# Kernel optimization log

Hardware: AMD Instinct MI355X
Metric: run time of the kernel (lower is better)

Reference implementation:

```python
import jax, jax.numpy as jnp
import numpy as np

HEADS = 2
HID = 128
IN_DIM = 128
OUT_DIM = 1
N_NODES = 50000
NEG_SLOPE = 0.2  # PyG GATConv default
EPS = 1e-16


def setup_inputs() -> dict:
    key = jax.random.key(0)
    ks = jax.random.split(key, 16)
    N, E = N_NODES, 800000
    x = jax.random.normal(ks[0], (N, IN_DIM), dtype=jnp.float32)
    edge_index = jax.random.randint(ks[1], (2, E), 0, N, dtype=jnp.int32)
    s = 0.1
    # GATConv 1: in=128 -> heads=2, out=128 per head
    W1 = jax.random.normal(ks[2], (IN_DIM, HEADS * HID), dtype=jnp.float32) * s
    a_src1 = jax.random.normal(ks[3], (HEADS, HID), dtype=jnp.float32) * s
    a_dst1 = jax.random.normal(ks[4], (HEADS, HID), dtype=jnp.float32) * s
    b1 = jnp.zeros((HEADS * HID,), dtype=jnp.float32)
    # GATConv 2: in=256 -> heads=2, out=128 per head
    W2 = jax.random.normal(ks[5], (HEADS * HID, HEADS * HID), dtype=jnp.float32) * s
    a_src2 = jax.random.normal(ks[6], (HEADS, HID), dtype=jnp.float32) * s
    a_dst2 = jax.random.normal(ks[7], (HEADS, HID), dtype=jnp.float32) * s
    b2 = jnp.zeros((HEADS * HID,), dtype=jnp.float32)
    # post_mp: Linear(256,128) -> Dropout -> Linear(128,1)
    Wp1 = jax.random.normal(ks[8], (HEADS * HID, HID), dtype=jnp.float32) * s
    bp1 = jnp.zeros((HID,), dtype=jnp.float32)
    Wp2 = jax.random.normal(ks[9], (HID, OUT_DIM), dtype=jnp.float32) * s
    bp2 = jnp.zeros((OUT_DIM,), dtype=jnp.float32)
    return {"x": x, "edge_index": edge_index,
            "W1": W1, "a_src1": a_src1, "a_dst1": a_dst1, "b1": b1,
            "W2": W2, "a_src2": a_src2, "a_dst2": a_dst2, "b2": b2,
            "Wp1": Wp1, "bp1": bp1, "Wp2": Wp2, "bp2": bp2}


def gat_conv(x, src, dst, W, a_src, a_dst, b, num_nodes):
    """PyG-style GATConv (concat=True). src/dst already include self-loops."""
    N = num_nodes
    h = (x @ W).reshape(N, HEADS, HID)                        # [N,H,C]
    alpha_s = jnp.einsum('nhc,hc->nh', h, a_src)              # [N,H]
    alpha_d = jnp.einsum('nhc,hc->nh', h, a_dst)              # [N,H]
    e = jax.nn.leaky_relu(alpha_s[src] + alpha_d[dst], NEG_SLOPE)  # [E,H]
    # segment softmax over destination node
    emax = jax.ops.segment_max(e, dst, num_segments=N)        # [N,H]
    emax = jnp.where(jnp.isfinite(emax), emax, 0.0)
    w = jnp.exp(e - emax[dst])                                # [E,H]
    denom = jax.ops.segment_sum(w, dst, num_segments=N)       # [N,H]
    alpha = w / (denom[dst] + EPS)                            # [E,H]
    out = jax.ops.segment_sum(h[src] * alpha[:, :, None], dst, num_segments=N)
    return out.reshape(N, HEADS * HID) + b


def reference(x, edge_index, W1, a_src1, a_dst1, b1, W2, a_src2, a_dst2, b2,
              Wp1, bp1, Wp2, bp2):
    N = x.shape[0]
    loops = jnp.arange(N, dtype=edge_index.dtype)
    src = jnp.concatenate([edge_index[0], loops])
    dst = jnp.concatenate([edge_index[1], loops])
    h = gat_conv(x, src, dst, W1, a_src1, a_dst1, b1, N)
    h = jax.nn.relu(h)  # dropout is identity in eval mode
    h = gat_conv(h, src, dst, W2, a_src2, a_dst2, b2, N)
    h = jax.nn.relu(h)
    h = h @ Wp1 + bp1
    h = h @ Wp2 + bp2
    return jax.nn.sigmoid(h)
```

## Files before the change

kernel.cpp:

```cpp
#include <hip/hip_runtime.h>

#define HID 128
#define C2 256
#define NEG 0.2f
#define L2E 1.44269504088896340736f

typedef __bf16 v8bf __attribute__((ext_vector_type(8)));
typedef float  v4f  __attribute__((ext_vector_type(4)));
typedef float  v2f  __attribute__((ext_vector_type(2)));
typedef unsigned short us8 __attribute__((ext_vector_type(8)));

__device__ __forceinline__ float bf2f(unsigned short u) {
    union { float f; unsigned int i; } v; v.i = ((unsigned int)u) << 16; return v.f;
}
__device__ __forceinline__ unsigned short f2bf(float f) {
    union { float f; unsigned int i; } v; v.f = f;
    unsigned int r = v.i + 0x7FFFu + ((v.i >> 16) & 1u);
    return (unsigned short)(r >> 16);
}
__device__ __forceinline__ float lrelu(float x) { return x > 0.f ? x : NEG * x; }

__device__ __forceinline__ void packB_body(const float* __restrict__ W,
                                           unsigned short* __restrict__ out,
                                           int K, int N, int idx) {
    int ksteps = K >> 5;
    int total = (N >> 4) * ksteps * 64;
    if (idx >= total) return;
    int lane = idx & 63;
    int rest = idx >> 6;
    int tt = rest / ksteps, k0 = rest - tt * ksteps;
    int n = (tt >> 3) * 128 + (lane & 15) * 8 + (tt & 7);
    int kb = k0 * 32 + (lane >> 4) * 8;
    us8 v;
#pragma unroll
    for (int j = 0; j < 8; ++j) v[j] = f2bf(W[(size_t)(kb + j) * N + n]);
    *(us8*)(out + (size_t)idx * 8) = v;
}

__global__ __launch_bounds__(256) void prep_kernel(const float* __restrict__ W1, unsigned short* W1p,
                                                   const float* __restrict__ W2, unsigned short* W2p,
                                                   const float* __restrict__ Wp1, unsigned short* Wp1p,
                                                   const int* __restrict__ ei, int* __restrict__ cnt,
                                                   int* __restrict__ rank, int E,
                                                   int b1, int b2, int b3) {
    int b = blockIdx.x;
    if (b < b1) { packB_body(W1, W1p, HID, C2, b * 256 + threadIdx.x); return; }
    b -= b1;
    if (b < b2) { packB_body(W2, W2p, C2, C2, b * 256 + threadIdx.x); return; }
    b -= b2;
    if (b < b3) { packB_body(Wp1, Wp1p, C2, HID, b * 256 + threadIdx.x); return; }
    b -= b3;
    int i = b * 256 + threadIdx.x;
    if (i >= E) return;
    int d = ei[E + i];
    rank[i] = atomicAdd(&cnt[d], 1);
}

__global__ __launch_bounds__(256) void scanA(const int* __restrict__ cnt, int* __restrict__ rs,
                                             int* __restrict__ part, int N) {
    __shared__ int s[256];
    int t = threadIdx.x, i = blockIdx.x * 256 + t;
    int v = (i < N) ? cnt[i] : 0;
    s[t] = v; __syncthreads();
    for (int off = 1; off < 256; off <<= 1) {
        int x = (t >= off) ? s[t - off] : 0;
        __syncthreads();
        s[t] += x;
        __syncthreads();
    }
    if (i < N) rs[i] = s[t] - v;
    if (t == 255) part[blockIdx.x] = s[255];
}

__global__ __launch_bounds__(256) void scanB(int* __restrict__ part, int n) {
    __shared__ int s[256];
    int t = threadIdx.x;
    int v = (t < n) ? part[t] : 0;
    s[t] = v; __syncthreads();
    for (int off = 1; off < 256; off <<= 1) {
        int x = (t >= off) ? s[t - off] : 0;
        __syncthreads();
        s[t] += x;
        __syncthreads();
    }
    if (t < n) part[t] = s[t] - v;
}

__global__ void scanC(int* __restrict__ rs, const int* __restrict__ part, int N, int E) {
    int i = blockIdx.x * 256 + threadIdx.x;
    if (i < N) rs[i] += part[blockIdx.x];
    if (i == 0) rs[N] = E;
}

template<bool AFP32, int G, int KSTEPS>
__global__ __launch_bounds__(256) void gemm_alpha(const void* __restrict__ Av,
                                                  const unsigned short* __restrict__ Bp,
                                                  const float* __restrict__ asrc,
                                                  const float* __restrict__ adst,
                                                  float* __restrict__ asd,
                                                  unsigned char* __restrict__ C,
                                                  int M, int N, int gemmBlocks,
                                                  const int* __restrict__ ei,
                                                  const int* __restrict__ rs,
                                                  const int* __restrict__ rank,
                                                  int* __restrict__ csr, int E) {
    if (blockIdx.x >= gemmBlocks) {
        int i = (blockIdx.x - gemmBlocks) * 256 + threadIdx.x;
        if (i < E) {
            int s = ei[i], d = ei[E + i];
            csr[rs[d] + rank[i]] = s;
        }
        return;
    }
    constexpr int K = KSTEPS * 32;
    int ngrp = N >> 7;
    int mtiles = M >> 4;
    int w = (blockIdx.x << 2) + (threadIdx.x >> 6);
    int groups = (mtiles + G - 1) / G;
    int mp = w / ngrp, g = w - mp * ngrp;
    if (mp >= groups) return;
    int lane = threadIdx.x & 63;
    int l16 = lane & 15, quad = lane >> 4;
    int mt0 = mp * G;

    int mrow[G];
#pragma unroll
    for (int gi = 0; gi < G; ++gi) {
        int mt = mt0 + gi;
        mrow[gi] = (mt < mtiles ? mt : mtiles - 1) * 16 + l16;
    }

    const unsigned short* Bf = Bp + ((size_t)(g * 8) * KSTEPS << 9) + lane * 8;
    v4f acc[G][8];
#pragma unroll
    for (int gi = 0; gi < G; ++gi)
#pragma unroll
        for (int t = 0; t < 8; ++t) acc[gi][t] = (v4f){0, 0, 0, 0};

#pragma unroll
    for (int k0 = 0; k0 < KSTEPS; ++k0) {
        v8bf bfr[8];
#pragma unroll
        for (int t = 0; t < 8; ++t)
            bfr[t] = *(const v8bf*)(Bf + ((size_t)(t * KSTEPS + k0) << 9));
        v8bf a[G];
        if (AFP32) {
            const float* A = (const float*)Av;
#pragma unroll
            for (int gi = 0; gi < G; ++gi) {
                const float* p = A + (size_t)mrow[gi] * K + k0 * 32 + quad * 8;
                float4 u0 = *(const float4*)p, u1 = *(const float4*)(p + 4);
                a[gi][0]=(__bf16)u0.x; a[gi][1]=(__bf16)u0.y; a[gi][2]=(__bf16)u0.z; a[gi][3]=(__bf16)u0.w;
                a[gi][4]=(__bf16)u1.x; a[gi][5]=(__bf16)u1.y; a[gi][6]=(__bf16)u1.z; a[gi][7]=(__bf16)u1.w;
            }
        } else {
            const unsigned short* A = (const unsigned short*)Av;
#pragma unroll
            for (int gi = 0; gi < G; ++gi)
                a[gi] = *(const v8bf*)(A + (size_t)mrow[gi] * K + k0 * 32 + quad * 8);
        }
#pragma unroll
        for (int t = 0; t < 8; ++t)
#pragma unroll
            for (int gi = 0; gi < G; ++gi)
                acc[gi][t] = __builtin_amdgcn_mfma_f32_16x16x32_bf16(a[gi], bfr[t], acc[gi][t], 0, 0, 0);
    }

    int n0 = g << 7;
    int cb = n0 + l16 * 8;
    float sv[8], dv[8];
#pragma unroll
    for (int t = 0; t < 8; ++t) {
        sv[t] = asrc[cb + t];
        dv[t] = adst[cb + t];
    }
#pragma unroll
    for (int gi = 0; gi < G; ++gi) {
        int mt = mt0 + gi;
        if (mt >= mtiles) break;
        int row0 = mt * 16 + quad * 4;
#pragma unroll
        for (int r = 0; r < 4; ++r) {
            float sa = 0.f, sd = 0.f;
#pragma unroll
            for (int t = 0; t < 8; ++t) {
                sa += acc[gi][t][r] * sv[t];
                sd += acc[gi][t][r] * dv[t];
            }
            unsigned int w0 = __builtin_amdgcn_cvt_pk_fp8_f32(acc[gi][0][r], acc[gi][1][r], 0, false);
            w0 = __builtin_amdgcn_cvt_pk_fp8_f32(acc[gi][2][r], acc[gi][3][r], w0, true);
            unsigned int w1 = __builtin_amdgcn_cvt_pk_fp8_f32(acc[gi][4][r], acc[gi][5][r], 0, false);
            w1 = __builtin_amdgcn_cvt_pk_fp8_f32(acc[gi][6][r], acc[gi][7][r], w1, true);
            *(uint2*)(C + (size_t)(row0 + r) * N + cb) = (uint2){w0, w1};
#pragma unroll
            for (int off = 8; off; off >>= 1) {
                sa += __shfl_xor(sa, off);
                sd += __shfl_xor(sd, off);
            }
            if (l16 == 0) {
                int row = row0 + r;
                asd[(size_t)row * 4 + g]     = sa * L2E;
                asd[(size_t)row * 4 + 2 + g] = sd * L2E;
            }
        }
    }
}

__global__ __launch_bounds__(256) void agg_kernel(const int* __restrict__ rs,
                                                  const int* __restrict__ csr,
                                                  const unsigned char* __restrict__ h,
                                                  const float* __restrict__ asd,
                                                  const float* __restrict__ bias,
                                                  unsigned short* __restrict__ out, int N) {
    int tid = threadIdx.x;
    int grp = tid >> 4;
    int sub = tid & 15;
    int d = blockIdx.x * 16 + grp;
    if (d >= N) return;
    int head = sub >> 3;
    int beg = rs[d], end = rs[d + 1];
    float adh = asd[(size_t)d * 4 + 2 + head];
    int cbase = sub * 16;
    const unsigned char* hc = h + cbase;
    v2f acc[8];
#pragma unroll
    for (int j = 0; j < 8; ++j) acc[j] = (v2f){0, 0};
    float den = 0.f;
#pragma unroll 2
    for (int i = beg; i < end; ++i) {
        int s = csr[i];
        float wgt = __builtin_amdgcn_exp2f(lrelu(asd[(size_t)s * 4 + head] + adh));
        den += wgt;
        uint4 u = *(const uint4*)(hc + ((size_t)s << 8));
        v2f w2 = {wgt, wgt};
        acc[0] += w2 * __builtin_amdgcn_cvt_pk_f32_fp8(u.x, false);
        acc[1] += w2 * __builtin_amdgcn_cvt_pk_f32_fp8(u.x, true);
        acc[2] += w2 * __builtin_amdgcn_cvt_pk_f32_fp8(u.y, false);
        acc[3] += w2 * __builtin_amdgcn_cvt_pk_f32_fp8(u.y, true);
        acc[4] += w2 * __builtin_amdgcn_cvt_pk_f32_fp8(u.z, false);
        acc[5] += w2 * __builtin_amdgcn_cvt_pk_f32_fp8(u.z, true);
        acc[6] += w2 * __builtin_amdgcn_cvt_pk_f32_fp8(u.w, false);
        acc[7] += w2 * __builtin_amdgcn_cvt_pk_f32_fp8(u.w, true);
    }
    float wS = __builtin_amdgcn_exp2f(lrelu(asd[(size_t)d * 4 + head] + adh));
    {
        uint4 u = *(const uint4*)(hc + ((size_t)d << 8));
        v2f wsv = {wS, wS};
        acc[0] += wsv * __builtin_amdgcn_cvt_pk_f32_fp8(u.x, false);
        acc[1] += wsv * __builtin_amdgcn_cvt_pk_f32_fp8(u.x, true);
        acc[2] += wsv * __builtin_amdgcn_cvt_pk_f32_fp8(u.y, false);
        acc[3] += wsv * __builtin_amdgcn_cvt_pk_f32_fp8(u.y, true);
        acc[4] += wsv * __builtin_amdgcn_cvt_pk_f32_fp8(u.z, false);
        acc[5] += wsv * __builtin_amdgcn_cvt_pk_f32_fp8(u.z, true);
        acc[6] += wsv * __builtin_amdgcn_cvt_pk_f32_fp8(u.w, false);
        acc[7] += wsv * __builtin_amdgcn_cvt_pk_f32_fp8(u.w, true);
    }
    float rden = 1.f / (den + wS + 1e-16f);
    us8 o0, o1;
#pragma unroll
    for (int j = 0; j < 4; ++j) {
        o0[2 * j]     = f2bf(fmaxf(acc[j].x * rden + bias[cbase + 2 * j], 0.f));
        o0[2 * j + 1] = f2bf(fmaxf(acc[j].y * rden + bias[cbase + 2 * j + 1], 0.f));
        o1[2 * j]     = f2bf(fmaxf(acc[4 + j].x * rden + bias[cbase + 8 + 2 * j], 0.f));
        o1[2 * j + 1] = f2bf(fmaxf(acc[4 + j].y * rden + bias[cbase + 8 + 2 * j + 1], 0.f));
    }
    *(us8*)(out + (size_t)d * C2 + cbase) = o0;
    *(us8*)(out + (size_t)d * C2 + cbase + 8) = o1;
}

template<int G, int KSTEPS>
__global__ __launch_bounds__(256) void gemm_final(const unsigned short* __restrict__ A,
                                                  const unsigned short* __restrict__ Bp,
                                                  const float* __restrict__ bp1,
                                                  const float* __restrict__ wp2,
                                                  const float* __restrict__ bp2,
                                                  float* __restrict__ out,
                                                  int M) {
    constexpr int K = KSTEPS * 32;
    int mtiles = M >> 4;
    int groups = (mtiles + G - 1) / G;
    int mp = (blockIdx.x << 2) + (threadIdx.x >> 6);
    if (mp >= groups) return;
    int lane = threadIdx.x & 63;
    int l16 = lane & 15, quad = lane >> 4;

    int mrow[G];
#pragma unroll
    for (int gi = 0; gi < G; ++gi) {
        int mt = mp * G + gi;
        mrow[gi] = (mt < mtiles ? mt : mtiles - 1) * 16 + l16;
    }

    const unsigned short* Bf = Bp + lane * 8;
    v4f acc[G][8];
#pragma unroll
    for (int gi = 0; gi < G; ++gi)
#pragma unroll
        for (int t = 0; t < 8; ++t) acc[gi][t] = (v4f){0, 0, 0, 0};
#pragma unroll
    for (int k0 = 0; k0 < KSTEPS; ++k0) {
        v8bf bfr[8];
#pragma unroll
        for (int t = 0; t < 8; ++t)
            bfr[t] = *(const v8bf*)(Bf + ((size_t)(t * KSTEPS + k0) << 9));
        v8bf a[G];
#pragma unroll
        for (int gi = 0; gi < G; ++gi)
            a[gi] = *(const v8bf*)(A + (size_t)mrow[gi] * K + k0 * 32 + quad * 8);
#pragma unroll
        for (int t = 0; t < 8; ++t)
#pragma unroll
            for (int gi = 0; gi < G; ++gi)
                acc[gi][t] = __builtin_amdgcn_mfma_f32_16x16x32_bf16(a[gi], bfr[t], acc[gi][t], 0, 0, 0);
    }
    int cb = l16 * 8;
    float wv8[8], bv[8];
#pragma unroll
    for (int t = 0; t < 8; ++t) {
        wv8[t] = wp2[cb + t];
        bv[t] = bp1[cb + t];
    }
    float bias2 = bp2[0];
#pragma unroll
    for (int gi = 0; gi < G; ++gi) {
        int mt = mp * G + gi;
        if (mt >= mtiles) break;
        int row0 = mt * 16 + quad * 4;
#pragma unroll
        for (int r = 0; r < 4; ++r) {
            float s = 0.f;
#pragma unroll
            for (int t = 0; t < 8; ++t) s += (acc[gi][t][r] + bv[t]) * wv8[t];
#pragma unroll
            for (int off = 8; off; off >>= 1) s += __shfl_xor(s, off);
            if (l16 == 0) {
                float xv = s + bias2;
                out[row0 + r] = 1.f / (1.f + __expf(-xv));
            }
        }
    }
}

extern "C" void kernel_launch(void* const* d_in, const int* in_sizes, int n_in,
                              void* d_out, int out_size, void* d_ws, size_t ws_size,
                              hipStream_t stream) {
    const float* x   = (const float*)d_in[0];
    const int*   ei  = (const int*)d_in[1];
    const float* W1  = (const float*)d_in[2];
    const float* as1 = (const float*)d_in[3];
    const float* ad1 = (const float*)d_in[4];
    const float* b1  = (const float*)d_in[5];
    const float* W2  = (const float*)d_in[6];
    const float* as2 = (const float*)d_in[7];
    const float* ad2 = (const float*)d_in[8];
    const float* b2  = (const float*)d_in[9];
    const float* Wp1 = (const float*)d_in[10];
    const float* bp1 = (const float*)d_in[11];
    const float* Wp2 = (const float*)d_in[12];
    const float* bp2 = (const float*)d_in[13];
    float* out = (float*)d_out;

    int NN = in_sizes[0] / HID;
    int E  = in_sizes[1] / 2;

    char* ws = (char*)d_ws;
    size_t off = 0;
    auto alloc = [&](size_t bytes) -> char* {
        char* p = ws + off;
        off += (bytes + 255) & ~(size_t)255;
        return p;
    };
    unsigned char*  bufH = (unsigned char*)alloc((size_t)NN * C2);
    unsigned short* bufO = (unsigned short*)alloc((size_t)NN * C2 * 2);
    float* asd = (float*)alloc((size_t)NN * 4 * sizeof(float));
    int* rs    = (int*)alloc((size_t)(NN + 1) * 4);
    int* cnt   = (int*)alloc((size_t)NN * 4);
    int* rank  = (int*)alloc((size_t)E * 4);
    int* csr   = (int*)alloc((size_t)E * 4);
    int* part  = (int*)alloc(1024);
    unsigned short* W1p  = (unsigned short*)alloc((size_t)HID * C2 * 2);
    unsigned short* W2p  = (unsigned short*)alloc((size_t)C2 * C2 * 2);
    unsigned short* Wp1p = (unsigned short*)alloc((size_t)C2 * HID * 2);

    int nchunk = (NN + 255) / 256;
    int eblk   = (E + 255) / 256;

    int pb1 = (HID * C2 / 8 + 255) / 256;
    int pb2 = (C2 * C2 / 8 + 255) / 256;
    int pb3 = (C2 * HID / 8 + 255) / 256;
    hipMemsetAsync(cnt, 0, (size_t)NN * 4, stream);
    prep_kernel<<<pb1 + pb2 + pb3 + eblk, 256, 0, stream>>>(W1, W1p, W2, W2p, Wp1, Wp1p,
                                                            ei, cnt, rank, E, pb1, pb2, pb3);
    scanA<<<nchunk, 256, 0, stream>>>(cnt, rs, part, NN);
    scanB<<<1, 256, 0, stream>>>(part, nchunk);
    scanC<<<nchunk, 256, 0, stream>>>(rs, part, NN, E);

    const int G = 2;
    int mtiles = NN / 16;
    int groups = (mtiles + G - 1) / G;
    int gemmBlocks = (groups * 2 + 3) / 4;
    int aggGrid = (NN + 15) / 16;

    gemm_alpha<true, G, 4><<<gemmBlocks + eblk, 256, 0, stream>>>(x, W1p, as1, ad1, asd, bufH,
                                                                  NN, C2, gemmBlocks,
                                                                  ei, rs, rank, csr, E);
    agg_kernel<<<aggGrid, 256, 0, stream>>>(rs, csr, bufH, asd, b1, bufO, NN);
    gemm_alpha<false, G, 8><<<gemmBlocks, 256, 0, stream>>>(bufO, W2p, as2, ad2, asd, bufH,
                                                            NN, C2, gemmBlocks,
                                                            nullptr, nullptr, nullptr, nullptr, 0);
    agg_kernel<<<aggGrid, 256, 0, stream>>>(rs, csr, bufH, asd, b2, bufO, NN);
    gemm_final<G, 8><<<(groups + 3) / 4, 256, 0, stream>>>(bufO, Wp1p, bp1, Wp2, bp2, out, NN);
}
```

Measured before the change: 298.1 us.

## Fuse GAT aggregation into following GEMMs via LDS and single-block scan

Each aggregation now writes its 64-row bf16 output tile to shared memory, and the next GEMM (layer-2 projection or the final MLP) consumes it in the same kernel. This removes the global round trip of the intermediate node features and two kernel launches. Separate buffers are used for the layer 1 and layer 2 features and attention scalars. The three-kernel prefix scan is replaced with one 1024-thread block doing a chunked serial scan, which cuts launches but serialises per-thread work and re-reads the counts.

```diff
diff --git a/kernel.cpp b/kernel.cpp
--- a/kernel.cpp
+++ b/kernel.cpp
@@ -56,40 +56,30 @@
     rank[i] = atomicAdd(&cnt[d], 1);
 }
 
-__global__ __launch_bounds__(256) void scanA(const int* __restrict__ cnt, int* __restrict__ rs,
-                                             int* __restrict__ part, int N) {
-    __shared__ int s[256];
-    int t = threadIdx.x, i = blockIdx.x * 256 + t;
-    int v = (i < N) ? cnt[i] : 0;
-    s[t] = v; __syncthreads();
-    for (int off = 1; off < 256; off <<= 1) {
-        int x = (t >= off) ? s[t - off] : 0;
+__global__ __launch_bounds__(1024) void scan_one(const int* __restrict__ cnt,
+                                                 int* __restrict__ rs, int N, int E) {
+    __shared__ int ls[1024];
+    int t = threadIdx.x;
+    int ch = (N + 1023) >> 10;
+    int base = t * ch;
+    int sum = 0;
+    for (int i = 0; i < ch; ++i) {
+        int idx = base + i;
+        sum += (idx < N) ? cnt[idx] : 0;
+    }
+    ls[t] = sum; __syncthreads();
+    for (int off = 1; off < 1024; off <<= 1) {
+        int x = (t >= off) ? ls[t - off] : 0;
         __syncthreads();
-        s[t] += x;
+        ls[t] += x;
         __syncthreads();
     }
-    if (i < N) rs[i] = s[t] - v;
-    if (t == 255) part[blockIdx.x] = s[255];
-}
-
-__global__ __launch_bounds__(256) void scanB(int* __restrict__ part, int n) {
-    __shared__ int s[256];
-    int t = threadIdx.x;
-    int v = (t < n) ? part[t] : 0;
-    s[t] = v; __syncthreads();
-    for (int off = 1; off < 256; off <<= 1) {
-        int x = (t >= off) ? s[t - off] : 0;
-        __syncthreads();
-        s[t] += x;
-        __syncthreads();
-    }
-    if (t < n) part[t] = s[t] - v;
-}
-
-__global__ void scanC(int* __restrict__ rs, const int* __restrict__ part, int N, int E) {
-    int i = blockIdx.x * 256 + threadIdx.x;
-    if (i < N) rs[i] += part[blockIdx.x];
-    if (i == 0) rs[N] = E;
+    int run = ls[t] - sum;
+    for (int i = 0; i < ch; ++i) {
+        int idx = base + i;
+        if (idx < N) { rs[idx] = run; run += cnt[idx]; }
+    }
+    if (t == 1023) rs[N] = E;
 }
 
 template<bool AFP32, int G, int KSTEPS>
@@ -206,97 +196,114 @@
     }
 }
 
-__global__ __launch_bounds__(256) void agg_kernel(const int* __restrict__ rs,
-                                                  const int* __restrict__ csr,
-                                                  const unsigned char* __restrict__ h,
-                                                  const float* __restrict__ asd,
-                                                  const float* __restrict__ bias,
-                                                  unsigned short* __restrict__ out, int N) {
-    int tid = threadIdx.x;
+__device__ __forceinline__ void agg_to_lds(const int* __restrict__ rs,
+                                           const int* __restrict__ csr,
+                                           const unsigned char* __restrict__ h,
+                                           const float* __restrict__ asd,
+                                           const float* __restrict__ bias,
+                                           unsigned short* __restrict__ sA,
+                                           int rowbase, int M, int tid) {
     int grp = tid >> 4;
     int sub = tid & 15;
-    int d = blockIdx.x * 16 + grp;
-    if (d >= N) return;
     int head = sub >> 3;
-    int beg = rs[d], end = rs[d + 1];
-    float adh = asd[(size_t)d * 4 + 2 + head];
     int cbase = sub * 16;
     const unsigned char* hc = h + cbase;
-    v2f acc[8];
-#pragma unroll
-    for (int j = 0; j < 8; ++j) acc[j] = (v2f){0, 0};
-    float den = 0.f;
+    for (int p = 0; p < 4; ++p) {
+        int d = rowbase + p * 16 + grp;
+        if (d >= M) continue;
+        int beg = rs[d], end = rs[d + 1];
+        float adh = asd[(size_t)d * 4 + 2 + head];
+        v2f acc[8];
+#pragma unroll
+        for (int j = 0; j < 8; ++j) acc[j] = (v2f){0, 0};
+        float den = 0.f;
 #pragma unroll 2
-    for (int i = beg; i < end; ++i) {
-        int s = csr[i];
-        float wgt = __builtin_amdgcn_exp2f(lrelu(asd[(size_t)s * 4 + head] + adh));
-        den += wgt;
-        uint4 u = *(const uint4*)(hc + ((size_t)s << 8));
-        v2f w2 = {wgt, wgt};
-        acc[0] += w2 * __builtin_amdgcn_cvt_pk_f32_fp8(u.x, false);
-        acc[1] += w2 * __builtin_amdgcn_cvt_pk_f32_fp8(u.x, true);
-        acc[2] += w2 * __builtin_amdgcn_cvt_pk_f32_fp8(u.y, false);
-        acc[3] += w2 * __builtin_amdgcn_cvt_pk_f32_fp8(u.y, true);
-        acc[4] += w2 * __builtin_amdgcn_cvt_pk_f32_fp8(u.z, false);
-        acc[5] += w2 * __builtin_amdgcn_cvt_pk_f32_fp8(u.z, true);
-        acc[6] += w2 * __builtin_amdgcn_cvt_pk_f32_fp8(u.w, false);
-        acc[7] += w2 * __builtin_amdgcn_cvt_pk_f32_fp8(u.w, true);
-    }
-    float wS = __builtin_amdgcn_exp2f(lrelu(asd[(size_t)d * 4 + head] + adh));
-    {
-        uint4 u = *(const uint4*)(hc + ((size_t)d << 8));
-        v2f wsv = {wS, wS};
-        acc[0] += wsv * __builtin_amdgcn_cvt_pk_f32_fp8(u.x, false);
-        acc[1] += wsv * __builtin_amdgcn_cvt_pk_f32_fp8(u.x, true);
-        acc[2] += wsv * __builtin_amdgcn_cvt_pk_f32_fp8(u.y, false);
-        acc[3] += wsv * __builtin_amdgcn_cvt_pk_f32_fp8(u.y, true);
-        acc[4] += wsv * __builtin_amdgcn_cvt_pk_f32_fp8(u.z, false);
-        acc[5] += wsv * __builtin_amdgcn_cvt_pk_f32_fp8(u.z, true);
-        acc[6] += wsv * __builtin_amdgcn_cvt_pk_f32_fp8(u.w, false);
-        acc[7] += wsv * __builtin_amdgcn_cvt_pk_f32_fp8(u.w, true);
-    }
-    float rden = 1.f / (den + wS + 1e-16f);
-    us8 o0, o1;
-#pragma unroll
-    for (int j = 0; j < 4; ++j) {
-        o0[2 * j]     = f2bf(fmaxf(acc[j].x * rden + bias[cbase + 2 * j], 0.f));
-        o0[2 * j + 1] = f2bf(fmaxf(acc[j].y * rden + bias[cbase + 2 * j + 1], 0.f));
-        o1[2 * j]     = f2bf(fmaxf(acc[4 + j].x * rden + bias[cbase + 8 + 2 * j], 0.f));
-        o1[2 * j + 1] = f2bf(fmaxf(acc[4 + j].y * rden + bias[cbase + 8 + 2 * j + 1], 0.f));
-    }
-    *(us8*)(out + (size_t)d * C2 + cbase) = o0;
-    *(us8*)(out + (size_t)d * C2 + cbase + 8) = o1;
-}
-
-template<int G, int KSTEPS>
-__global__ __launch_bounds__(256) void gemm_final(const unsigned short* __restrict__ A,
-                                                  const unsigned short* __restrict__ Bp,
-                                                  const float* __restrict__ bp1,
-                                                  const float* __restrict__ wp2,
-                                                  const float* __restrict__ bp2,
-                                                  float* __restrict__ out,
-                                                  int M) {
-    constexpr int K = KSTEPS * 32;
+        for (int i = beg; i < end; ++i) {
+            int s = csr[i];
+            float wgt = __builtin_amdgcn_exp2f(lrelu(asd[(size_t)s * 4 + head] + adh));
+            den += wgt;
+            uint4 u = *(const uint4*)(hc + ((size_t)s << 8));
+            v2f w2 = {wgt, wgt};
+            acc[0] += w2 * __builtin_amdgcn_cvt_pk_f32_fp8(u.x, false);
+            acc[1] += w2 * __builtin_amdgcn_cvt_pk_f32_fp8(u.x, true);
+            acc[2] += w2 * __builtin_amdgcn_cvt_pk_f32_fp8(u.y, false);
+            acc[3] += w2 * __builtin_amdgcn_cvt_pk_f32_fp8(u.y, true);
+            acc[4] += w2 * __builtin_amdgcn_cvt_pk_f32_fp8(u.z, false);
+            acc[5] += w2 * __builtin_amdgcn_cvt_pk_f32_fp8(u.z, true);
+            acc[6] += w2 * __builtin_amdgcn_cvt_pk_f32_fp8(u.w, false);
+            acc[7] += w2 * __builtin_amdgcn_cvt_pk_f32_fp8(u.w, true);
+        }
+        float wS = __builtin_amdgcn_exp2f(lrelu(asd[(size_t)d * 4 + head] + adh));
+        {
+            uint4 u = *(const uint4*)(hc + ((size_t)d << 8));
+            v2f wsv = {wS, wS};
+            acc[0] += wsv * __builtin_amdgcn_cvt_pk_f32_fp8(u.x, false);
+            acc[1] += wsv * __builtin_amdgcn_cvt_pk_f32_fp8(u.x, true);
+            acc[2] += wsv * __builtin_amdgcn_cvt_pk_f32_fp8(u.y, false);
+            acc[3] += wsv * __builtin_amdgcn_cvt_pk_f32_fp8(u.y, true);
+            acc[4] += wsv * __builtin_amdgcn_cvt_pk_f32_fp8(u.z, false);
+            acc[5] += wsv * __builtin_amdgcn_cvt_pk_f32_fp8(u.z, true);
+            acc[6] += wsv * __builtin_amdgcn_cvt_pk_f32_fp8(u.w, false);
+            acc[7] += wsv * __builtin_amdgcn_cvt_pk_f32_fp8(u.w, true);
+        }
+        float rden = 1.f / (den + wS + 1e-16f);
+        us8 o0, o1;
+#pragma unroll
+        for (int j = 0; j < 4; ++j) {
+            o0[2 * j]     = f2bf(fmaxf(acc[j].x * rden + bias[cbase + 2 * j], 0.f));
+            o0[2 * j + 1] = f2bf(fmaxf(acc[j].y * rden + bias[cbase + 2 * j + 1], 0.f));
+            o1[2 * j]     = f2bf(fmaxf(acc[4 + j].x * rden + bias[cbase + 8 + 2 * j], 0.f));
+            o1[2 * j + 1] = f2bf(fmaxf(acc[4 + j].y * rden + bias[cbase + 8 + 2 * j + 1], 0.f));
+        }
+        unsigned short* dst = sA + (size_t)(p * 16 + grp) * C2 + cbase;
+        *(us8*)dst = o0;
+        *(us8*)(dst + 8) = o1;
+    }
+}
+
+template<int KSTEPS>
+__global__ __launch_bounds__(256) void agg_gemm_alpha(const int* __restrict__ rs,
+                                                      const int* __restrict__ csr,
+                                                      const unsigned char* __restrict__ hIn,
+                                                      const float* __restrict__ asdIn,
+                                                      const float* __restrict__ biasIn,
+                                                      const unsigned short* __restrict__ Bp,
+                                                      const float* __restrict__ asrc,
+                                                      const float* __restrict__ adst,
+                                                      float* __restrict__ asdOut,
+                                                      unsigned char* __restrict__ C,
+                                                      int M, int N) {
+    __shared__ __align__(16) unsigned short sA[64 * C2];
+    int tid = threadIdx.x;
+    int rowbase = blockIdx.x * 64;
+    agg_to_lds(rs, csr, hIn, asdIn, biasIn, sA, rowbase, M, tid);
+    __syncthreads();
+
+    constexpr int G = 2;
+    int ngrp = N >> 7;
     int mtiles = M >> 4;
+    int w = (blockIdx.x << 2) + (tid >> 6);
     int groups = (mtiles + G - 1) / G;
-    int mp = (blockIdx.x << 2) + (threadIdx.x >> 6);
+    int mp = w / ngrp, g = w - mp * ngrp;
     if (mp >= groups) return;
-    int lane = threadIdx.x & 63;
+    int lane = tid & 63;
     int l16 = lane & 15, quad = lane >> 4;
-
-    int mrow[G];
+    int mt0 = mp * G;
+
+    int lrow[G];
 #pragma unroll
     for (int gi = 0; gi < G; ++gi) {
-        int mt = mp * G + gi;
-        mrow[gi] = (mt < mtiles ? mt : mtiles - 1) * 16 + l16;
-    }
-
-    const unsigned short* Bf = Bp + lane * 8;
+        int mt = mt0 + gi;
+        lrow[gi] = (mt < mtiles ? mt : mtiles - 1) * 16 + l16 - rowbase;
+    }
+
+    const unsigned short* Bf = Bp + ((size_t)(g * 8) * KSTEPS << 9) + lane * 8;
     v4f acc[G][8];
 #pragma unroll
     for (int gi = 0; gi < G; ++gi)
 #pragma unroll
         for (int t = 0; t < 8; ++t) acc[gi][t] = (v4f){0, 0, 0, 0};
+
 #pragma unroll
     for (int k0 = 0; k0 < KSTEPS; ++k0) {
         v8bf bfr[8];
@@ -306,12 +313,93 @@
         v8bf a[G];
 #pragma unroll
         for (int gi = 0; gi < G; ++gi)
-            a[gi] = *(const v8bf*)(A + (size_t)mrow[gi] * K + k0 * 32 + quad * 8);
+            a[gi] = *(const v8bf*)(sA + (size_t)lrow[gi] * C2 + k0 * 32 + quad * 8);
 #pragma unroll
         for (int t = 0; t < 8; ++t)
 #pragma unroll
             for (int gi = 0; gi < G; ++gi)
                 acc[gi][t] = __builtin_amdgcn_mfma_f32_16x16x32_bf16(a[gi], bfr[t], acc[gi][t], 0, 0, 0);
+    }
+
+    int n0 = g << 7;
+    int cb = n0 + l16 * 8;
+    float sv[8], dv[8];
+#pragma unroll
+    for (int t = 0; t < 8; ++t) {
+        sv[t] = asrc[cb + t];
+        dv[t] = adst[cb + t];
+    }
+#pragma unroll
+    for (int gi = 0; gi < G; ++gi) {
+        int mt = mt0 + gi;
+        if (mt >= mtiles) break;
+        int row0 = mt * 16 + quad * 4;
+#pragma unroll
+        for (int r = 0; r < 4; ++r) {
+            float sa = 0.f, sd = 0.f;
+#pragma unroll
+            for (int t = 0; t < 8; ++t) {
+                sa += acc[gi][t][r] * sv[t];
+                sd += acc[gi][t][r] * dv[t];
+            }
+            unsigned int w0 = __builtin_amdgcn_cvt_pk_fp8_f32(acc[gi][0][r], acc[gi][1][r], 0, false);
+            w0 = __builtin_amdgcn_cvt_pk_fp8_f32(acc[gi][2][r], acc[gi][3][r], w0, true);
+            unsigned int w1 = __builtin_amdgcn_cvt_pk_fp8_f32(acc[gi][4][r], acc[gi][5][r], 0, false);
+            w1 = __builtin_amdgcn_cvt_pk_fp8_f32(acc[gi][6][r], acc[gi][7][r], w1, true);
+            *(uint2*)(C + (size_t)(row0 + r) * N + cb) = (uint2){w0, w1};
+#pragma unroll
+            for (int off = 8; off; off >>= 1) {
+                sa += __shfl_xor(sa, off);
+                sd += __shfl_xor(sd, off);
+            }
+            if (l16 == 0) {
+                int row = row0 + r;
+                asdOut[(size_t)row * 4 + g]     = sa * L2E;
+                asdOut[(size_t)row * 4 + 2 + g] = sd * L2E;
+            }
+        }
+    }
+}
+
+template<int KSTEPS>
+__global__ __launch_bounds__(256) void agg_gemm_final(const int* __restrict__ rs,
+                                                      const int* __restrict__ csr,
+                                                      const unsigned char* __restrict__ hIn,
+                                                      const float* __restrict__ asdIn,
+                                                      const float* __restrict__ biasIn,
+                                                      const unsigned short* __restrict__ Bp,
+                                                      const float* __restrict__ bp1,
+                                                      const float* __restrict__ wp2,
+                                                      const float* __restrict__ bp2,
+                                                      float* __restrict__ out,
+                                                      int M) {
+    __shared__ __align__(16) unsigned short sA[64 * C2];
+    int tid = threadIdx.x;
+    int rowbase = blockIdx.x * 64;
+    agg_to_lds(rs, csr, hIn, asdIn, biasIn, sA, rowbase, M, tid);
+    __syncthreads();
+
+    int mtiles = M >> 4;
+    int mp = (blockIdx.x << 2) + (tid >> 6);
+    if (mp >= mtiles) return;
+    int lane = tid & 63;
+    int l16 = lane & 15, quad = lane >> 4;
+    int lrow = mp * 16 + l16 - rowbase;
+
+    const unsigned short* Bf = Bp + lane * 8;
+    v4f acc[8];
+#pragma unroll
+    for (int t = 0; t < 8; ++t) acc[t] = (v4f){0, 0, 0, 0};
+#pragma unroll
+    for (int k0 = 0; k0 < KSTEPS; ++k0) {
+        v8bf bfr[8];
+#pragma unroll
+        for (int t = 0; t < 8; ++t)
+            bfr[t] = *(const v8bf*)(Bf + ((size_t)(t * KSTEPS + k0) << 9));
+        v8bf a = *(const v8bf*)(sA + (size_t)lrow * C2 + k0 * 32 + quad * 8);
+#pragma unroll
+        for (int t = 0; t < 8; ++t)
+            acc[t] = __builtin_amdgcn_mfma_f32_16x16x32_bf16(a, bfr[t], acc[t], 0, 0, 0);
     }
     int cb = l16 * 8;
     float wv8[8], bv[8];
@@ -321,22 +409,17 @@
         bv[t] = bp1[cb + t];
     }
     float bias2 = bp2[0];
-#pragma unroll
-    for (int gi = 0; gi < G; ++gi) {
-        int mt = mp * G + gi;
-        if (mt >= mtiles) break;
-        int row0 = mt * 16 + quad * 4;
-#pragma unroll
-        for (int r = 0; r < 4; ++r) {
-            float s = 0.f;
-#pragma unroll
-            for (int t = 0; t < 8; ++t) s += (acc[gi][t][r] + bv[t]) * wv8[t];
-#pragma unroll
-            for (int off = 8; off; off >>= 1) s += __shfl_xor(s, off);
-            if (l16 == 0) {
-                float xv = s + bias2;
-                out[row0 + r] = 1.f / (1.f + __expf(-xv));
-            }
+    int row0 = mp * 16 + quad * 4;
+#pragma unroll
+    for (int r = 0; r < 4; ++r) {
+        float s = 0.f;
+#pragma unroll
+        for (int t = 0; t < 8; ++t) s += (acc[t][r] + bv[t]) * wv8[t];
+#pragma unroll
+        for (int off = 8; off; off >>= 1) s += __shfl_xor(s, off);
+        if (l16 == 0) {
+            float xv = s + bias2;
+            out[row0 + r] = 1.f / (1.f + __expf(-xv));
         }
     }
 }
@@ -370,20 +453,19 @@
         off += (bytes + 255) & ~(size_t)255;
         return p;
     };
-    unsigned char*  bufH = (unsigned char*)alloc((size_t)NN * C2);
-    unsigned short* bufO = (unsigned short*)alloc((size_t)NN * C2 * 2);
-    float* asd = (float*)alloc((size_t)NN * 4 * sizeof(float));
+    unsigned char*  bufH1 = (unsigned char*)alloc((size_t)NN * C2);
+    unsigned char*  bufH2 = (unsigned char*)alloc((size_t)NN * C2);
+    float* asd1 = (float*)alloc((size_t)NN * 4 * sizeof(float));
+    float* asd2 = (float*)alloc((size_t)NN * 4 * sizeof(float));
     int* rs    = (int*)alloc((size_t)(NN + 1) * 4);
     int* cnt   = (int*)alloc((size_t)NN * 4);
     int* rank  = (int*)alloc((size_t)E * 4);
     int* csr   = (int*)alloc((size_t)E * 4);
-    int* part  = (int*)alloc(1024);
     unsigned short* W1p  = (unsigned short*)alloc((size_t)HID * C2 * 2);
     unsigned short* W2p  = (unsigned short*)alloc((size_t)C2 * C2 * 2);
     unsigned short* Wp1p = (unsigned short*)alloc((size_t)C2 * HID * 2);
 
-    int nchunk = (NN + 255) / 256;
-    int eblk   = (E + 255) / 256;
+    int eblk = (E + 255) / 256;
 
     int pb1 = (HID * C2 / 8 + 255) / 256;
     int pb2 = (C2 * C2 / 8 + 255) / 256;
@@ -391,23 +473,20 @@
     hipMemsetAsync(cnt, 0, (size_t)NN * 4, stream);
     prep_kernel<<<pb1 + pb2 + pb3 + eblk, 256, 0, stream>>>(W1, W1p, W2, W2p, Wp1, Wp1p,
                                                             ei, cnt, rank, E, pb1, pb2, pb3);
-    scanA<<<nchunk, 256, 0, stream>>>(cnt, rs, part, NN);
-    scanB<<<1, 256, 0, stream>>>(part, nchunk);
-    scanC<<<nchunk, 256, 0, stream>>>(rs, part, NN, E);
+    scan_one<<<1, 1024, 0, stream>>>(cnt, rs, NN, E);
 
     const int G = 2;
     int mtiles = NN / 16;
     int groups = (mtiles + G - 1) / G;
     int gemmBlocks = (groups * 2 + 3) / 4;
-    int aggGrid = (NN + 15) / 16;
-
-    gemm_alpha<true, G, 4><<<gemmBlocks + eblk, 256, 0, stream>>>(x, W1p, as1, ad1, asd, bufH,
+    int fuseGrid = gemmBlocks;
+    int finGrid  = (mtiles + 3) / 4;
+
+    gemm_alpha<true, G, 4><<<gemmBlocks + eblk, 256, 0, stream>>>(x, W1p, as1, ad1, asd1, bufH1,
                                                                   NN, C2, gemmBlocks,
                                                                   ei, rs, rank, csr, E);
-    agg_kernel<<<aggGrid, 256, 0, stream>>>(rs, csr, bufH, asd, b1, bufO, NN);
-    gemm_alpha<false, G, 8><<<gemmBlocks, 256, 0, stream>>>(bufO, W2p, as2, ad2, asd, bufH,
-                                                            NN, C2, gemmBlocks,
-                                                            nullptr, nullptr, nullptr, nullptr, 0);
-    agg_kernel<<<aggGrid, 256, 0, stream>>>(rs, csr, bufH, asd, b2, bufO, NN);
-    gemm_final<G, 8><<<(groups + 3) / 4, 256, 0, stream>>>(bufO, Wp1p, bp1, Wp2, bp2, out, NN);
-}
+    agg_gemm_alpha<8><<<fuseGrid, 256, 0, stream>>>(rs, csr, bufH1, asd1, b1,
+                                                    W2p, as2, ad2, asd2, bufH2, NN, C2);
+    agg_gemm_final<8><<<finGrid, 256, 0, stream>>>(rs, csr, bufH2, asd2, b2,
+                                                   Wp1p, bp1, Wp2, bp2, out, NN);
+}
```

Result: slower. 400.1 us (+34.2%).

## Collapse three-kernel scan into one block and set GEMM group size to one

Applied to the files above, without the earlier changes.

Replaces the three-pass prefix scan (scanA/scanB/scanC) with a single 1024-thread block. Each thread serially sums a strided chunk of counts, the block scans the partial sums, and each thread writes its chunk's offsets. This removes two kernel launches and the partials buffer, at the cost of a serial single-block pass over 50k counts. It also changes the GEMM tile grouping G from 2 to 1, which doubles the block count for the GEMM and final kernels and exposes more parallelism at the cost of less reuse per block.

```diff
diff --git a/kernel.cpp b/kernel.cpp
--- a/kernel.cpp
+++ b/kernel.cpp
@@ -56,40 +56,30 @@
     rank[i] = atomicAdd(&cnt[d], 1);
 }
 
-__global__ __launch_bounds__(256) void scanA(const int* __restrict__ cnt, int* __restrict__ rs,
-                                             int* __restrict__ part, int N) {
-    __shared__ int s[256];
-    int t = threadIdx.x, i = blockIdx.x * 256 + t;
-    int v = (i < N) ? cnt[i] : 0;
-    s[t] = v; __syncthreads();
-    for (int off = 1; off < 256; off <<= 1) {
-        int x = (t >= off) ? s[t - off] : 0;
+__global__ __launch_bounds__(1024) void scan_one(const int* __restrict__ cnt,
+                                                 int* __restrict__ rs, int N, int E) {
+    __shared__ int ls[1024];
+    int t = threadIdx.x;
+    int ch = (N + 1023) >> 10;
+    int base = t * ch;
+    int sum = 0;
+    for (int i = 0; i < ch; ++i) {
+        int idx = base + i;
+        sum += (idx < N) ? cnt[idx] : 0;
+    }
+    ls[t] = sum; __syncthreads();
+    for (int off = 1; off < 1024; off <<= 1) {
+        int x = (t >= off) ? ls[t - off] : 0;
         __syncthreads();
-        s[t] += x;
+        ls[t] += x;
         __syncthreads();
     }
-    if (i < N) rs[i] = s[t] - v;
-    if (t == 255) part[blockIdx.x] = s[255];
-}
-
-__global__ __launch_bounds__(256) void scanB(int* __restrict__ part, int n) {
-    __shared__ int s[256];
-    int t = threadIdx.x;
-    int v = (t < n) ? part[t] : 0;
-    s[t] = v; __syncthreads();
-    for (int off = 1; off < 256; off <<= 1) {
-        int x = (t >= off) ? s[t - off] : 0;
-        __syncthreads();
-        s[t] += x;
-        __syncthreads();
-    }
-    if (t < n) part[t] = s[t] - v;
-}
-
-__global__ void scanC(int* __restrict__ rs, const int* __restrict__ part, int N, int E) {
-    int i = blockIdx.x * 256 + threadIdx.x;
-    if (i < N) rs[i] += part[blockIdx.x];
-    if (i == 0) rs[N] = E;
+    int run = ls[t] - sum;
+    for (int i = 0; i < ch; ++i) {
+        int idx = base + i;
+        if (idx < N) { rs[idx] = run; run += cnt[idx]; }
+    }
+    if (t == 1023) rs[N] = E;
 }
 
 template<bool AFP32, int G, int KSTEPS>
@@ -377,13 +367,11 @@
     int* cnt   = (int*)alloc((size_t)NN * 4);
     int* rank  = (int*)alloc((size_t)E * 4);
     int* csr   = (int*)alloc((size_t)E * 4);
-    int* part  = (int*)alloc(1024);
     unsigned short* W1p  = (unsigned short*)alloc((size_t)HID * C2 * 2);
     unsigned short* W2p  = (unsigned short*)alloc((size_t)C2 * C2 * 2);
     unsigned short* Wp1p = (unsigned short*)alloc((size_t)C2 * HID * 2);
 
-    int nchunk = (NN + 255) / 256;
-    int eblk   = (E + 255) / 256;
+    int eblk = (E + 255) / 256;
 
     int pb1 = (HID * C2 / 8 + 255) / 256;
     int pb2 = (C2 * C2 / 8 + 255) / 256;
@@ -391,15 +379,14 @@
     hipMemsetAsync(cnt, 0, (size_t)NN * 4, stream);
     prep_kernel<<<pb1 + pb2 + pb3 + eblk, 256, 0, stream>>>(W1, W1p, W2, W2p, Wp1, Wp1p,
                                                             ei, cnt, rank, E, pb1, pb2, pb3);
-    scanA<<<nchunk, 256, 0, stream>>>(cnt, rs, part, NN);
-    scanB<<<1, 256, 0, stream>>>(part, nchunk);
-    scanC<<<nchunk, 256, 0, stream>>>(rs, part, NN, E);
-
-    const int G = 2;
+    scan_one<<<1, 1024, 0, stream>>>(cnt, rs, NN, E);
+
+    const int G = 1;
     int mtiles = NN / 16;
-    int groups = (mtiles + G - 1) / G;
+    int groups = mtiles;
     int gemmBlocks = (groups * 2 + 3) / 4;
     int aggGrid = (NN + 15) / 16;
+    int finGrid = (mtiles + 3) / 4;
 
     gemm_alpha<true, G, 4><<<gemmBlocks + eblk, 256, 0, stream>>>(x, W1p, as1, ad1, asd, bufH,
                                                                   NN, C2, gemmBlocks,
@@ -409,5 +396,5 @@
                                                             NN, C2, gemmBlocks,
                                                             nullptr, nullptr, nullptr, nullptr, 0);
     agg_kernel<<<aggGrid, 256, 0, stream>>>(rs, csr, bufH, asd, b2, bufO, NN);
-    gemm_final<G, 8><<<(groups + 3) / 4, 256, 0, stream>>>(bufO, Wp1p, bp1, Wp2, bp2, out, NN);
-}
+    gemm_final<G, 8><<<finGrid, 256, 0, stream>>>(bufO, Wp1p, bp1, Wp2, bp2, out, NN);
+}
```

Measured after the change: 359.0 us. 1.2x slower.
